# Optimization experiments

Measured on AMD Instinct MI355X. Metric: run time of the kernel, lower is better.

Reference implementation:

```python
import jax, jax.numpy as jnp
import numpy as np

TOP_K = 4
EPS = 1e-6


def setup_inputs() -> dict:
    key = jax.random.key(0)
    k1, k2, k3 = jax.random.split(key, 3)
    B, Q, N, H, W = 4, 200, 32, 256, 256
    pred_masks = jax.random.normal(k1, (B, Q, H, W), dtype=jnp.float32)
    pred_logits = jax.random.normal(k2, (B, Q, 2), dtype=jnp.float32)
    gt_masks = (jax.random.uniform(k3, (B, N, H, W)) < 0.3).astype(jnp.float32)
    return {"pred_masks": pred_masks, "pred_logits": pred_logits, "gt_masks": gt_masks}


def _combined_scores(pred_masks, pred_logits, gt_masks):
    """IoU * class-score, shape [B, Q, N]."""
    pm = jax.nn.sigmoid(pred_masks)                    # [B,Q,H,W]
    cls = jax.nn.softmax(pred_logits, axis=-1)[..., 1]  # [B,Q]
    B, Q = pm.shape[:2]
    N = gt_masks.shape[1]
    pmf = pm.reshape(B, Q, -1)                         # [B,Q,D]
    tmf = gt_masks.reshape(B, N, -1)                   # [B,N,D]
    inter = jnp.einsum('bqd,bnd->bqn', pmf, tmf)
    union = pmf.sum(-1)[:, :, None] + tmf.sum(-1)[:, None, :] - inter
    iou = inter / (union + EPS)
    return iou * cls[:, :, None]


def _greedy_assign(combined):
    """Greedy per-GT top-k with dedup. combined: [Q,N] -> sel indices [N,k], -1 = dropped."""
    Q = combined.shape[0]
    k = min(TOP_K, Q)

    def step(assigned, col):
        _, idx = jax.lax.top_k(col, k)          # [k] query indices for this GT
        taken = assigned[idx]                   # already assigned -> drop
        sel = jnp.where(taken, -1, idx)
        assigned = assigned.at[idx].set(True)
        return assigned, sel

    _, sels = jax.lax.scan(step, jnp.zeros(Q, dtype=bool), combined.T)
    return sels  # [N, k]


def reference(pred_masks, pred_logits, gt_masks):
    combined = _combined_scores(pred_masks, pred_logits, gt_masks)  # [B,Q,N]
    sels = jax.vmap(_greedy_assign)(combined)                       # [B,N,k]
    B, N, k = sels.shape
    src_idx = sels
    tgt_idx = jnp.broadcast_to(jnp.arange(N, dtype=jnp.int32)[None, :, None], sels.shape)
    valid = sels >= 0
    tgt_idx = jnp.where(valid, tgt_idx, -1)
    return src_idx, tgt_idx, valid
```

## Files before the change

kernel.cpp:

```cpp
#include <hip/hip_runtime.h>
#include <math.h>
#include <stdint.h>

#define BB    4
#define QQ    200
#define NGT   32
#define DD    65536
#define TOPK  4
#define EPSF  1e-6f
#define QP    208

#define QT16  13
#define KG    32
#define KSPAN (DD / KG)
#define BK    256
#define NCH   (KSPAN / BK)

typedef float  f32x4  __attribute__((ext_vector_type(4)));
typedef __bf16 bf16x8 __attribute__((ext_vector_type(8)));

#define PERM_HI16 0x07060302u
#define PERM_LO16 0x05040100u

#define RAW_BARRIER() asm volatile("s_barrier" ::: "memory")
#define VM_DRAIN()    asm volatile("s_waitcnt vmcnt(0)" ::: "memory")

#define GLOAD_LDS16(gptr, lptr)                                                  \
    __builtin_amdgcn_global_load_lds(                                            \
        (const __attribute__((address_space(1))) uint32_t*)(gptr),               \
        (__attribute__((address_space(3))) uint32_t*)(lptr), 16, 0, 0)

__global__ __launch_bounds__(256) void k_pack(const float* __restrict__ gt,
                                              uint32_t* __restrict__ packed,
                                              float* __restrict__ zero_base) {
    int zidx = blockIdx.x * 256 + threadIdx.x;
    if (zidx < BB * NGT * QP + BB * QP) zero_base[zidx] = 0.0f;

    int blk = blockIdx.x;
    int b = blk >> 6;
    int d0 = ((blk & 63) * 256 + threadIdx.x) * 4;
    uint32_t px = 0, py = 0, pz = 0, pw = 0;
    const float* gb = gt + (size_t)b * NGT * DD + d0;
#pragma unroll
    for (int n = 0; n < NGT; ++n) {
        float4 g = *(const float4*)(gb + (size_t)n * DD);
        px |= (g.x > 0.5f ? 1u : 0u) << n;
        py |= (g.y > 0.5f ? 1u : 0u) << n;
        pz |= (g.z > 0.5f ? 1u : 0u) << n;
        pw |= (g.w > 0.5f ? 1u : 0u) << n;
    }
    *(uint4*)(packed + (size_t)b * DD + d0) = make_uint4(px, py, pz, pw);
}

__global__ __launch_bounds__(256) void k_tsum(const uint32_t* __restrict__ packed,
                                              float* __restrict__ tsum) {
    int b = blockIdx.x >> 5;
    int n = blockIdx.x & 31;
    const uint4* pp = (const uint4*)(packed + (size_t)b * DD);
    int cnt = 0;
    for (int i = threadIdx.x; i < DD / 4; i += 256) {
        uint4 w = pp[i];
        cnt += (int)((w.x >> n) & 1u) + (int)((w.y >> n) & 1u) +
               (int)((w.z >> n) & 1u) + (int)((w.w >> n) & 1u);
    }
#pragma unroll
    for (int off = 32; off; off >>= 1) cnt += __shfl_xor(cnt, off);
    __shared__ int red[4];
    if ((threadIdx.x & 63) == 0) red[threadIdx.x >> 6] = cnt;
    __syncthreads();
    if (threadIdx.x == 0)
        tsum[blockIdx.x] = (float)(red[0] + red[1] + red[2] + red[3]);
}

__global__ __launch_bounds__(256) void k_mfma(const float* __restrict__ pm,
                                              const uint32_t* __restrict__ packed,
                                              float* __restrict__ inter,
                                              float* __restrict__ psum) {
    int blk = blockIdx.x;
    int b   = blk / (QT16 * KG);
    int rem = blk % (QT16 * KG);
    int qt  = rem / KG;
    int kg  = rem % KG;
    int tid = threadIdx.x, lane = tid & 63, wave = tid >> 6;
    int m = lane & 15, quad = lane >> 4;

    __shared__ float sA[2][16][BK];

    const float*    pmb = pm + (size_t)b * QQ * DD + (size_t)kg * KSPAN;
    const uint32_t* pkb = packed + (size_t)b * DD + (size_t)kg * KSPAN;

    int row0 = wave * 4;
    int qrow[4];
#pragma unroll
    for (int i = 0; i < 4; ++i) {
        int qg = qt * 16 + row0 + i;
        qrow[i] = qg < QQ ? qg : QQ - 1;
    }

    f32x4 cH0 = {0.f,0.f,0.f,0.f}, cL0 = {0.f,0.f,0.f,0.f};
    f32x4 cH1 = {0.f,0.f,0.f,0.f}, cL1 = {0.f,0.f,0.f,0.f};
    float ps = 0.f;

#pragma unroll
    for (int i = 0; i < 4; ++i) {
        int r = row0 + i;
        const float* gsrc = pmb + (size_t)qrow[i] * DD + ((lane ^ (r & 7)) << 2);
        GLOAD_LDS16(gsrc, &sA[0][r][0]);
    }
    VM_DRAIN();
    RAW_BARRIER();

    for (int c = 0; c < NCH; ++c) {
        int buf = c & 1;
        if (c + 1 < NCH) {
#pragma unroll
            for (int i = 0; i < 4; ++i) {
                int r = row0 + i;
                const float* gsrc = pmb + (size_t)qrow[i] * DD
                                        + (size_t)(c + 1) * BK + ((lane ^ (r & 7)) << 2);
                GLOAD_LDS16(gsrc, &sA[buf ^ 1][r][0]);
            }
        }

#pragma unroll
        for (int st = 0; st < 2; ++st) {
            int k0 = wave * 64 + st * 32 + quad * 8;
            int c0 = k0 >> 2;
            float4 a0 = *(const float4*)&sA[buf][m][(c0 ^ (m & 7)) << 2];
            float4 a1 = *(const float4*)&sA[buf][m][((c0 + 1) ^ (m & 7)) << 2];
            const uint32_t* bpc = pkb + (size_t)c * BK + k0;
            uint4 w0 = *(const uint4*)(bpc);
            uint4 w1 = *(const uint4*)(bpc + 4);

            float xs[8] = {a0.x, a0.y, a0.z, a0.w, a1.x, a1.y, a1.z, a1.w};
            uint32_t hu[8], mu[8], lu[8];
#pragma unroll
            for (int i = 0; i < 8; ++i) {
                float x  = xs[i];
                float sg = __builtin_amdgcn_rcpf(1.0f + __expf(-x));
                ps += sg;
                uint32_t u0 = __float_as_uint(sg);
                float hi = __uint_as_float(u0 & 0xFFFF0000u);
                float r1 = sg - hi;
                uint32_t u1 = __float_as_uint(r1);
                float mi = __uint_as_float(u1 & 0xFFFF0000u);
                float r2 = r1 - mi;
                hu[i] = u0; mu[i] = u1; lu[i] = __float_as_uint(r2);
            }
            union { uint4 u; bf16x8 v; } ah, am, al;
            ah.u = make_uint4(__builtin_amdgcn_perm(hu[1], hu[0], PERM_HI16),
                              __builtin_amdgcn_perm(hu[3], hu[2], PERM_HI16),
                              __builtin_amdgcn_perm(hu[5], hu[4], PERM_HI16),
                              __builtin_amdgcn_perm(hu[7], hu[6], PERM_HI16));
            am.u = make_uint4(__builtin_amdgcn_perm(mu[1], mu[0], PERM_HI16),
                              __builtin_amdgcn_perm(mu[3], mu[2], PERM_HI16),
                              __builtin_amdgcn_perm(mu[5], mu[4], PERM_HI16),
                              __builtin_amdgcn_perm(mu[7], mu[6], PERM_HI16));
            al.u = make_uint4(__builtin_amdgcn_perm(lu[1], lu[0], PERM_HI16),
                              __builtin_amdgcn_perm(lu[3], lu[2], PERM_HI16),
                              __builtin_amdgcn_perm(lu[5], lu[4], PERM_HI16),
                              __builtin_amdgcn_perm(lu[7], lu[6], PERM_HI16));

            uint32_t wj[8] = {w0.x, w0.y, w0.z, w0.w, w1.x, w1.y, w1.z, w1.w};
            uint32_t ob[8];
#pragma unroll
            for (int j = 0; j < 8; ++j) {
                uint32_t t = wj[j] >> m;
                ob[j] = (t & 0x10001u) * 0x3F80u;
            }
            union { uint4 u; bf16x8 v; } b0, b1;
            b0.u = make_uint4(__builtin_amdgcn_perm(ob[1], ob[0], PERM_LO16),
                              __builtin_amdgcn_perm(ob[3], ob[2], PERM_LO16),
                              __builtin_amdgcn_perm(ob[5], ob[4], PERM_LO16),
                              __builtin_amdgcn_perm(ob[7], ob[6], PERM_LO16));
            b1.u = make_uint4(__builtin_amdgcn_perm(ob[1], ob[0], PERM_HI16),
                              __builtin_amdgcn_perm(ob[3], ob[2], PERM_HI16),
                              __builtin_amdgcn_perm(ob[5], ob[4], PERM_HI16),
                              __builtin_amdgcn_perm(ob[7], ob[6], PERM_HI16));

            cH0 = __builtin_amdgcn_mfma_f32_16x16x32_bf16(ah.v, b0.v, cH0, 0, 0, 0);
            cL0 = __builtin_amdgcn_mfma_f32_16x16x32_bf16(am.v, b0.v, cL0, 0, 0, 0);
            cL0 = __builtin_amdgcn_mfma_f32_16x16x32_bf16(al.v, b0.v, cL0, 0, 0, 0);
            cH1 = __builtin_amdgcn_mfma_f32_16x16x32_bf16(ah.v, b1.v, cH1, 0, 0, 0);
            cL1 = __builtin_amdgcn_mfma_f32_16x16x32_bf16(am.v, b1.v, cL1, 0, 0, 0);
            cL1 = __builtin_amdgcn_mfma_f32_16x16x32_bf16(al.v, b1.v, cL1, 0, 0, 0);
        }

        if (c + 1 < NCH) VM_DRAIN();
        RAW_BARRIER();
    }

    ps += __shfl_xor(ps, 16);
    ps += __shfl_xor(ps, 32);
    if (lane < 16) {
        int qg = qt * 16 + m;
        if (qg < QQ) atomicAdd(&psum[b * QP + qg], ps);
    }

    float c8[8];
#pragma unroll
    for (int r = 0; r < 4; ++r) {
        c8[r]     = cH0[r] + cL0[r];
        c8[4 + r] = cH1[r] + cL1[r];
    }
    __syncthreads();
    float* cred = (float*)sA;
    if (wave > 0) {
        float* dst = cred + ((wave - 1) * 64 + lane) * 9;
#pragma unroll
        for (int r = 0; r < 8; ++r) dst[r] = c8[r];
    }
    __syncthreads();
    if (wave == 0) {
#pragma unroll
        for (int wv = 0; wv < 3; ++wv) {
            const float* sp = cred + (wv * 64 + lane) * 9;
#pragma unroll
            for (int r = 0; r < 8; ++r) c8[r] += sp[r];
        }
#pragma unroll
        for (int r = 0; r < 4; ++r) {
            int qg = qt * 16 + quad * 4 + r;
            if (qg < QQ) {
                atomicAdd(&inter[(b * NGT + m) * QP + qg],      c8[r]);
                atomicAdd(&inter[(b * NGT + 16 + m) * QP + qg], c8[4 + r]);
            }
        }
    }
}

__global__ __launch_bounds__(256) void k_match(const float* __restrict__ inter,
                                               const float* __restrict__ psum,
                                               const float* __restrict__ tsum,
                                               const float* __restrict__ logits,
                                               int* __restrict__ out) {
    int b = blockIdx.x;
    int tid = threadIdx.x, lane = tid & 63, wave = tid >> 6;
    __shared__ int sidx[NGT][TOPK];

    for (int nn = 0; nn < 8; ++nn) {
        int n  = wave * 8 + nn;
        int bn = b * NGT + n;
        float tsn = tsum[bn];
        float v[4];
#pragma unroll
        for (int s = 0; s < 4; ++s) {
            int q = lane + 64 * s;
            if (q < QQ) {
                float iv = inter[(size_t)bn * QP + q];
                float un = psum[b * QP + q] + tsn - iv;
                float l0 = logits[(b * QQ + q) * 2];
                float l1 = logits[(b * QQ + q) * 2 + 1];
                float cl = 1.0f / (1.0f + expf(l0 - l1));
                v[s] = iv / (un + EPSF) * cl;
            } else {
                v[s] = -INFINITY;
            }
        }
        for (int k = 0; k < TOPK; ++k) {
            float bv = -INFINITY;
            int   bi = 0x7fffffff;
#pragma unroll
            for (int s = 0; s < 4; ++s)
                if (v[s] > bv) { bv = v[s]; bi = lane + 64 * s; }
#pragma unroll
            for (int off = 32; off; off >>= 1) {
                float ov = __shfl_xor(bv, off);
                int   oi = __shfl_xor(bi, off);
                if (ov > bv || (ov == bv && oi < bi)) { bv = ov; bi = oi; }
            }
            if (lane == (bi & 63)) v[bi >> 6] = -INFINITY;
            if (lane == 0) sidx[n][k] = bi;
        }
    }
    __syncthreads();

    if (wave == 0) {
        int* src = out;
        int* tgt = out + BB * NGT * TOPK;
        int* val = out + 2 * BB * NGT * TOPK;
        int asg = 0;
        for (int n = 0; n < NGT; ++n) {
            int ids[4] = {sidx[n][0], sidx[n][1], sidx[n][2], sidx[n][3]};
            int newasg = asg;
#pragma unroll
            for (int k = 0; k < TOPK; ++k) {
                int idx = ids[k];
                int owner = idx & 63, slot = idx >> 6;
                int oasg = __shfl(asg, owner);
                int taken = (oasg >> slot) & 1;
                if (lane == owner) newasg |= (1 << slot);
                if (lane == 0) {
                    int o = (b * NGT + n) * TOPK + k;
                    src[o] = taken ? -1 : idx;
                    tgt[o] = taken ? -1 : n;
                    val[o] = taken ? 0 : 1;
                }
            }
            asg = newasg;
        }
    }
}

extern "C" void kernel_launch(void* const* d_in, const int* in_sizes, int n_in,
                              void* d_out, int out_size, void* d_ws, size_t ws_size,
                              hipStream_t stream) {
    const float* pred_masks  = (const float*)d_in[0];
    const float* pred_logits = (const float*)d_in[1];
    const float* gt_masks    = (const float*)d_in[2];

    uint8_t* ws = (uint8_t*)d_ws;
    uint32_t* packed = (uint32_t*)ws;
    float* tsum  = (float*)(ws + (size_t)BB * DD * 4);
    float* inter = tsum + BB * NGT;
    float* psum  = inter + BB * NGT * QP;

    k_pack <<<BB * (DD / 1024), 256, 0, stream>>>(gt_masks, packed, inter);
    k_tsum <<<BB * NGT,         256, 0, stream>>>(packed, tsum);
    k_mfma <<<BB * QT16 * KG,   256, 0, stream>>>(pred_masks, packed, inter, psum);
    k_match<<<BB,               256, 0, stream>>>(inter, psum, tsum, pred_logits, (int*)d_out);
}
```

Before: 363.8 us.

## Fuse GT-sum and matching into MFMA kernel via last-block completion

Removes the separate tsum and match kernels. GT foreground counts are now computed inside the qt==0 MFMA blocks using ballot/popcount with atomic accumulation. The matching and greedy dedup run in the last block to finish, detected with an atomic done counter. This saves two kernel launches and their inter-kernel gaps, but makes the matching stage serial within one block and reads partial sums through atomics.

```diff
diff --git a/kernel.cpp b/kernel.cpp
--- a/kernel.cpp
+++ b/kernel.cpp
@@ -15,6 +15,8 @@
 #define KSPAN (DD / KG)
 #define BK    256
 #define NCH   (KSPAN / BK)
+#define NWG2  (BB * QT16 * KG)
+#define ZCNT  (BB*NGT + BB*NGT*QP + BB*QP + 1)
 
 typedef float  f32x4  __attribute__((ext_vector_type(4)));
 typedef __bf16 bf16x8 __attribute__((ext_vector_type(8)));
@@ -34,7 +36,7 @@
                                               uint32_t* __restrict__ packed,
                                               float* __restrict__ zero_base) {
     int zidx = blockIdx.x * 256 + threadIdx.x;
-    if (zidx < BB * NGT * QP + BB * QP) zero_base[zidx] = 0.0f;
+    if (zidx < ZCNT) zero_base[zidx] = 0.0f;
 
     int blk = blockIdx.x;
     int b = blk >> 6;
@@ -52,30 +54,14 @@
     *(uint4*)(packed + (size_t)b * DD + d0) = make_uint4(px, py, pz, pw);
 }
 
-__global__ __launch_bounds__(256) void k_tsum(const uint32_t* __restrict__ packed,
-                                              float* __restrict__ tsum) {
-    int b = blockIdx.x >> 5;
-    int n = blockIdx.x & 31;
-    const uint4* pp = (const uint4*)(packed + (size_t)b * DD);
-    int cnt = 0;
-    for (int i = threadIdx.x; i < DD / 4; i += 256) {
-        uint4 w = pp[i];
-        cnt += (int)((w.x >> n) & 1u) + (int)((w.y >> n) & 1u) +
-               (int)((w.z >> n) & 1u) + (int)((w.w >> n) & 1u);
-    }
-#pragma unroll
-    for (int off = 32; off; off >>= 1) cnt += __shfl_xor(cnt, off);
-    __shared__ int red[4];
-    if ((threadIdx.x & 63) == 0) red[threadIdx.x >> 6] = cnt;
-    __syncthreads();
-    if (threadIdx.x == 0)
-        tsum[blockIdx.x] = (float)(red[0] + red[1] + red[2] + red[3]);
-}
-
 __global__ __launch_bounds__(256) void k_mfma(const float* __restrict__ pm,
                                               const uint32_t* __restrict__ packed,
                                               float* __restrict__ inter,
-                                              float* __restrict__ psum) {
+                                              float* __restrict__ psum,
+                                              float* __restrict__ tsum,
+                                              const float* __restrict__ logits,
+                                              int* __restrict__ done,
+                                              int* __restrict__ out) {
     int blk = blockIdx.x;
     int b   = blk / (QT16 * KG);
     int rem = blk % (QT16 * KG);
@@ -88,6 +74,20 @@
 
     const float*    pmb = pm + (size_t)b * QQ * DD + (size_t)kg * KSPAN;
     const uint32_t* pkb = packed + (size_t)b * DD + (size_t)kg * KSPAN;
+
+    if (qt == 0) {
+        uint32_t w8[8];
+#pragma unroll
+        for (int j = 0; j < 8; ++j) w8[j] = pkb[tid + 256 * j];
+#pragma unroll
+        for (int n = 0; n < NGT; ++n) {
+            int c = 0;
+#pragma unroll
+            for (int j = 0; j < 8; ++j)
+                c += __popcll(__ballot((w8[j] >> n) & 1u));
+            if (lane == 0) atomicAdd(&tsum[b * NGT + n], (float)c);
+        }
+    }
 
     int row0 = wave * 4;
     int qrow[4];
@@ -227,61 +227,67 @@
             }
         }
     }
-}
-
-__global__ __launch_bounds__(256) void k_match(const float* __restrict__ inter,
-                                               const float* __restrict__ psum,
-                                               const float* __restrict__ tsum,
-                                               const float* __restrict__ logits,
-                                               int* __restrict__ out) {
-    int b = blockIdx.x;
-    int tid = threadIdx.x, lane = tid & 63, wave = tid >> 6;
-    __shared__ int sidx[NGT][TOPK];
-
-    for (int nn = 0; nn < 8; ++nn) {
-        int n  = wave * 8 + nn;
-        int bn = b * NGT + n;
-        float tsn = tsum[bn];
-        float v[4];
+
+    int* lflag = (int*)sA + 4096;
+    int* sidxb = (int*)sA + 2048;
+    __syncthreads();
+    __threadfence();
+    if (tid == 0) {
+        int t = atomicAdd(done, 1);
+        *lflag = (t == NWG2 - 1) ? 1 : 0;
+    }
+    __syncthreads();
+    if (*lflag) {
+        __threadfence();
+        int mb = wave;
+        float tsn_l = (lane < NGT) ? atomicAdd(&tsum[mb * NGT + lane], 0.0f) : 0.f;
+        float psq[4], cls[4];
 #pragma unroll
         for (int s = 0; s < 4; ++s) {
             int q = lane + 64 * s;
             if (q < QQ) {
-                float iv = inter[(size_t)bn * QP + q];
-                float un = psum[b * QP + q] + tsn - iv;
-                float l0 = logits[(b * QQ + q) * 2];
-                float l1 = logits[(b * QQ + q) * 2 + 1];
-                float cl = 1.0f / (1.0f + expf(l0 - l1));
-                v[s] = iv / (un + EPSF) * cl;
-            } else {
-                v[s] = -INFINITY;
-            }
-        }
-        for (int k = 0; k < TOPK; ++k) {
-            float bv = -INFINITY;
-            int   bi = 0x7fffffff;
-#pragma unroll
-            for (int s = 0; s < 4; ++s)
-                if (v[s] > bv) { bv = v[s]; bi = lane + 64 * s; }
-#pragma unroll
-            for (int off = 32; off; off >>= 1) {
-                float ov = __shfl_xor(bv, off);
-                int   oi = __shfl_xor(bi, off);
-                if (ov > bv || (ov == bv && oi < bi)) { bv = ov; bi = oi; }
-            }
-            if (lane == (bi & 63)) v[bi >> 6] = -INFINITY;
-            if (lane == 0) sidx[n][k] = bi;
-        }
-    }
-    __syncthreads();
-
-    if (wave == 0) {
+                psq[s] = atomicAdd(&psum[mb * QP + q], 0.0f);
+                float l0 = logits[(mb * QQ + q) * 2];
+                float l1 = logits[(mb * QQ + q) * 2 + 1];
+                cls[s] = 1.0f / (1.0f + expf(l0 - l1));
+            } else { psq[s] = 0.f; cls[s] = 0.f; }
+        }
+        int* sidxw = sidxb + mb * NGT * TOPK;
+        for (int n = 0; n < NGT; ++n) {
+            float tsn = __shfl(tsn_l, n);
+            float v[4];
+#pragma unroll
+            for (int s = 0; s < 4; ++s) {
+                int q = lane + 64 * s;
+                if (q < QQ) {
+                    float iv = atomicAdd(&inter[((size_t)mb * NGT + n) * QP + q], 0.0f);
+                    float un = psq[s] + tsn - iv;
+                    v[s] = iv / (un + EPSF) * cls[s];
+                } else v[s] = -INFINITY;
+            }
+            for (int k = 0; k < TOPK; ++k) {
+                float bv = -INFINITY;
+                int   bi = 0x7fffffff;
+#pragma unroll
+                for (int s = 0; s < 4; ++s)
+                    if (v[s] > bv) { bv = v[s]; bi = lane + 64 * s; }
+#pragma unroll
+                for (int off = 32; off; off >>= 1) {
+                    float ov = __shfl_xor(bv, off);
+                    int   oi = __shfl_xor(bi, off);
+                    if (ov > bv || (ov == bv && oi < bi)) { bv = ov; bi = oi; }
+                }
+                if (lane == (bi & 63)) v[bi >> 6] = -INFINITY;
+                if (lane == 0) sidxw[n * TOPK + k] = bi;
+            }
+        }
+        __syncthreads();
         int* src = out;
         int* tgt = out + BB * NGT * TOPK;
         int* val = out + 2 * BB * NGT * TOPK;
         int asg = 0;
         for (int n = 0; n < NGT; ++n) {
-            int ids[4] = {sidx[n][0], sidx[n][1], sidx[n][2], sidx[n][3]};
+            int ids[4] = {sidxw[n * 4], sidxw[n * 4 + 1], sidxw[n * 4 + 2], sidxw[n * 4 + 3]};
             int newasg = asg;
 #pragma unroll
             for (int k = 0; k < TOPK; ++k) {
@@ -291,7 +297,7 @@
                 int taken = (oasg >> slot) & 1;
                 if (lane == owner) newasg |= (1 << slot);
                 if (lane == 0) {
-                    int o = (b * NGT + n) * TOPK + k;
+                    int o = (mb * NGT + n) * TOPK + k;
                     src[o] = taken ? -1 : idx;
                     tgt[o] = taken ? -1 : n;
                     val[o] = taken ? 0 : 1;
@@ -314,9 +320,9 @@
     float* tsum  = (float*)(ws + (size_t)BB * DD * 4);
     float* inter = tsum + BB * NGT;
     float* psum  = inter + BB * NGT * QP;
-
-    k_pack <<<BB * (DD / 1024), 256, 0, stream>>>(gt_masks, packed, inter);
-    k_tsum <<<BB * NGT,         256, 0, stream>>>(packed, tsum);
-    k_mfma <<<BB * QT16 * KG,   256, 0, stream>>>(pred_masks, packed, inter, psum);
-    k_match<<<BB,               256, 0, stream>>>(inter, psum, tsum, pred_logits, (int*)d_out);
+    int*   done  = (int*)(psum + BB * QP);
+
+    k_pack<<<BB * (DD / 1024), 256, 0, stream>>>(gt_masks, packed, tsum);
+    k_mfma<<<NWG2, 256, 0, stream>>>(pred_masks, packed, inter, psum, tsum,
+                                     pred_logits, done, (int*)d_out);
 }
```

Result: slower. 704.0 us (+93.5%).
